# Optimization experiments

Measured on AMD Instinct MI355X. Metric: run time of the kernel, lower is better.

## Reference

```python
import jax, jax.numpy as jnp
import numpy as np

T, B, TD, HD, VD = 64, 4096, 512, 256, 484
LN_EPS = 1e-5   # torch nn.LayerNorm default
COS_EPS = 1e-8  # torch F.cosine_similarity default


def setup_inputs() -> dict:
    key = jax.random.key(0)
    ks = jax.random.split(key, 6)
    w = lambda k, shape: jax.random.normal(k, shape, dtype=jnp.float32) * 0.02
    return {
        "t_feat": jax.random.normal(ks[0], (B, TD), dtype=jnp.float32),
        "W1": w(ks[1], (T, HD, TD)),            # torch Linear weight layout [out, in]
        "b1": w(ks[2], (T, HD)),
        "gamma": jnp.ones((T, HD), jnp.float32),
        "beta": jnp.zeros((T, HD), jnp.float32),
        "W2": w(ks[3], (T, VD, HD)),
        "b2": w(ks[4], (T, VD)),
        "centroids": jax.random.normal(ks[5], (T, VD), dtype=jnp.float32),
    }


def reference(t_feat, W1, b1, gamma, beta, W2, b2, centroids):
    # All T per-task mappers batched into one grouped GEMM pipeline.
    # Linear1: [B, TD] x [T, HD, TD] -> [T, B, HD]
    h = jnp.einsum("bd,thd->tbh", t_feat, W1) + b1[:, None, :]
    # LayerNorm over hidden dim (per task affine params)
    mu = jnp.mean(h, axis=-1, keepdims=True)
    var = jnp.mean(jnp.square(h - mu), axis=-1, keepdims=True)
    h = (h - mu) * jax.lax.rsqrt(var + LN_EPS) * gamma[:, None, :] + beta[:, None, :]
    # Exact GELU (torch nn.GELU default uses erf)
    h = jax.nn.gelu(h, approximate=False)
    # Linear2: [T, B, HD] x [T, VD, HD] -> [T, B, VD] predicted visual features
    v = jnp.einsum("tbh,tvh->tbv", h, W2) + b2[:, None, :]
    # Cosine similarity vs each task centroid (eps-clamped norms, as in torch)
    v_norm = jnp.maximum(jnp.linalg.norm(v, axis=-1), COS_EPS)          # [T, B]
    c_norm = jnp.maximum(jnp.linalg.norm(centroids, axis=-1), COS_EPS)  # [T]
    cos = jnp.einsum("tbv,tv->tb", v, centroids) / (v_norm * c_norm[:, None])
    distances = jnp.mean(1.0 - cos, axis=-1)  # [T] mean cosine distance per task
    best_task = jnp.argmin(distances)          # top-1 routing decision
    return distances, best_task
```

## Files before the change

kernel.cpp:

```cpp
#include <hip/hip_runtime.h>
#include <math.h>

#define TASKS 64
#define NB    4096
#define TDI   512
#define HDI   256
#define VDI   484

#define WS_TF   ((size_t)0)
#define WS_W1   ((size_t)4194304)
#define WS_W2   ((size_t)20971520)
#define WS_CN   ((size_t)37748736)
#define WS_BC   ((size_t)37748992)
#define WS_ACC  ((size_t)37749248)

#define LDS_HP 0
#define LDS_B2 32768
#define LDS_R0 34816
#define LDS_R1 35840
#define LDS_MU 36864
#define LDS_RS 37120
#define SMEM_BYTES 37376

typedef _Float16 half8 __attribute__((ext_vector_type(8)));
typedef float    f32x4 __attribute__((ext_vector_type(4)));

#define MFMA16(a, b, c) __builtin_amdgcn_mfma_f32_16x16x32_f16((a), (b), (c), 0, 0, 0)

__device__ __forceinline__ float gelu_exact(float x) {
  float az = fabsf(x) * 0.70710678118654752f;
  float d  = fmaf(0.3275911f, az, 1.0f);
  float t; asm("v_rcp_f32 %0, %1" : "=v"(t) : "v"(d));
  float p  = fmaf(t, 1.061405429f, -1.453152027f);
  p = fmaf(t, p, 1.421413741f);
  p = fmaf(t, p, -0.284496736f);
  p = fmaf(t, p, 0.254829592f);
  p = p * t;
  float m = az * az * -1.4426950408889634f;
  float e; asm("v_exp_f32 %0, %1" : "=v"(e) : "v"(m));
  float er = fmaf(-p, e, 1.0f);
  er = copysignf(er, x);
  float hx = 0.5f * x;
  return fmaf(hx, er, hx);
}

extern "C" __global__ void prep_all(const float* __restrict__ t_feat,
                                    const float* __restrict__ W1,
                                    const float* __restrict__ W2,
                                    const float* __restrict__ b2,
                                    const float* __restrict__ cent,
                                    _Float16* __restrict__ tf,
                                    _Float16* __restrict__ w1,
                                    _Float16* __restrict__ w2,
                                    float* __restrict__ cnorm,
                                    float* __restrict__ bc,
                                    float* __restrict__ accum) {
  __shared__ __align__(16) char pbuf[17408];
  const int bid = blockIdx.x, tid = threadIdx.x;

  if (bid < 2304) {
    const float* src;
    half8* dst;
    int w2vdBase = -1;

    if (bid < 256) {
      int rb = bid >> 2, kq = bid & 3;
      src = t_feat + (size_t)rb * 64 * 512 + kq * 128;
      dst = (half8*)tf + ((size_t)rb * 4096 + kq * 1024);
    } else if (bid < 1280) {
      int g = bid - 256;
      int t = g >> 4, w_ = (g >> 2) & 3, kq = g & 3;
      src = W1 + ((size_t)t * 256 + w_ * 64) * 512 + kq * 128;
      dst = (half8*)w1 + ((size_t)t * 16384 + w_ * 4096 + kq * 1024);
    } else {
      int g = bid - 1280;
      int t = g >> 4, sub = g & 15;
      int p = sub >> 3, w_ = (sub >> 1) & 3, kq = sub & 1;
      src = W2 + (size_t)t * 484 * 256 + kq * 128;
      w2vdBase = p * 256 + w_ * 64;
      dst = (half8*)w2 + ((size_t)t * 16384 + p * 8192 + w_ * 2048 + kq * 1024);
    }

    const int srcStride = (w2vdBase < 0) ? 512 : 256;
    ushort* lds = (ushort*)pbuf;
    #pragma unroll
    for (int j = 0; j < 8; ++j) {
      int f = j * 256 + tid;
      int row = f >> 5, kc = f & 31;
      float4 v = make_float4(0.f, 0.f, 0.f, 0.f);
      if (w2vdBase < 0) {
        v = ((const float4*)(src + (size_t)row * srcStride))[kc];
      } else {
        int vd = w2vdBase + row;
        if (vd < VDI) v = ((const float4*)(src + (size_t)vd * 256))[kc];
      }
      _Float16 h4[4] = {(_Float16)v.x, (_Float16)v.y, (_Float16)v.z, (_Float16)v.w};
      *(ushort4*)(&lds[row * 136 + kc * 4]) = *(const ushort4*)h4;
    }
    __syncthreads();

    #pragma unroll
    for (int j = 0; j < 4; ++j) {
      int u = j * 256 + tid;
      int ksl = u >> 8, rg = (u >> 6) & 3, q = (u >> 4) & 3, l15 = u & 15;
      int row = rg * 16 + l15, k8l = ksl * 4 + q;
      half8 val = *(const half8*)(pbuf + row * 272 + k8l * 16);
      if (w2vdBase >= 0 && (w2vdBase + row) == VDI) continue;
      dst[u] = val;
    }
  } else {
    int t = bid - 2304;
    int h = tid;
    float* redc = (float*)pbuf;
    float* redb = (float*)(pbuf + 1024);
    float wcv = 0.f;
    for (int v = 0; v < VDI; ++v)
      wcv += W2[((size_t)t * VDI + v) * HDI + h] * cent[(size_t)t * VDI + v];
    {
      int ks = h >> 5, q = (h >> 3) & 3;
      size_t o = (size_t)t * 16384 + 8192 + 3 * 2048 + ks * 256 + 2 * 64 + q * 16 + 4;
      w2[o * 8 + (h & 7)] = (_Float16)wcv;
    }
    float c2 = 0.f, b2c = 0.f;
    for (int v = h; v < VDI; v += 256) {
      float c = cent[(size_t)t * VDI + v];
      c2 += c * c;
      b2c += b2[(size_t)t * VDI + v] * c;
    }
    redc[tid] = c2; redb[tid] = b2c;
    __syncthreads();
    if (tid < 64) {
      c2  = redc[tid] + redc[tid + 64] + redc[tid + 128] + redc[tid + 192];
      b2c = redb[tid] + redb[tid + 64] + redb[tid + 128] + redb[tid + 192];
      #pragma unroll
      for (int off = 32; off; off >>= 1) { c2 += __shfl_xor(c2, off); b2c += __shfl_xor(b2c, off); }
      if (tid == 0) { cnorm[t] = sqrtf(c2); bc[t] = b2c; accum[t] = 0.f; }
    }
  }
}


#define STEP_RELOAD(A, ACC, PB) do {                                           \
  __builtin_amdgcn_s_setprio(1);                                               \
  _Pragma("unroll") for (int ct_ = 0; ct_ < 4; ++ct_) {                        \
    ACC[0][ct_] = MFMA16(A[0], b[ct_], ACC[0][ct_]);                           \
    ACC[1][ct_] = MFMA16(A[1], b[ct_], ACC[1][ct_]);                           \
    ACC[2][ct_] = MFMA16(A[2], b[ct_], ACC[2][ct_]);                           \
    ACC[3][ct_] = MFMA16(A[3], b[ct_], ACC[3][ct_]);                           \
    b[ct_] = (PB)[ct_ * 64];                                                   \
  }                                                                            \
  __builtin_amdgcn_s_setprio(0);                                               \
} while (0)

#define STEP_LAST(A, ACC) do {                                                 \
  __builtin_amdgcn_s_setprio(1);                                               \
  _Pragma("unroll") for (int ct_ = 0; ct_ < 4; ++ct_) {                        \
    ACC[0][ct_] = MFMA16(A[0], b[ct_], ACC[0][ct_]);                           \
    ACC[1][ct_] = MFMA16(A[1], b[ct_], ACC[1][ct_]);                           \
    ACC[2][ct_] = MFMA16(A[2], b[ct_], ACC[2][ct_]);                           \
    ACC[3][ct_] = MFMA16(A[3], b[ct_], ACC[3][ct_]);                           \
  }                                                                            \
  __builtin_amdgcn_s_setprio(0);                                               \
} while (0)

#define LD_A4(D, P) do { D[0] = (P)[0]; D[1] = (P)[64]; D[2] = (P)[128]; D[3] = (P)[192]; } while (0)

#define P3_STEP(ACC, HN) do {                                                  \
  __builtin_amdgcn_s_setprio(1);                                               \
  ACC[0][0]=MFMA16(a0[0],b[0],ACC[0][0]); ACC[1][0]=MFMA16(a0[1],b[0],ACC[1][0]); \
  ACC[2][0]=MFMA16(a0[2],b[0],ACC[2][0]); ACC[3][0]=MFMA16(a0[3],b[0],ACC[3][0]); \
  b[0]=pc[0];                                                                  \
  ACC[0][1]=MFMA16(a0[0],b[1],ACC[0][1]); ACC[1][1]=MFMA16(a0[1],b[1],ACC[1][1]); \
  ACC[2][1]=MFMA16(a0[2],b[1],ACC[2][1]); ACC[3][1]=MFMA16(a0[3],b[1],ACC[3][1]); \
  b[1]=pc[64];                                                                 \
  ACC[0][2]=MFMA16(a0[0],b[2],ACC[0][2]); ACC[1][2]=MFMA16(a0[1],b[2],ACC[1][2]); \
  ACC[2][2]=MFMA16(a0[2],b[2],ACC[2][2]); ACC[3][2]=MFMA16(a0[3],b[2],ACC[3][2]); \
  b[2]=pc[128];                                                                \
  ACC[0][3]=MFMA16(a0[0],b[3],ACC[0][3]); a0[0]=*(const half8*)(HN);           \
  ACC[1][3]=MFMA16(a0[1],b[3],ACC[1][3]); a0[1]=*(const half8*)((HN)+1024);    \
  ACC[2][3]=MFMA16(a0[2],b[3],ACC[2][3]); a0[2]=*(const half8*)((HN)+2048);    \
  ACC[3][3]=MFMA16(a0[3],b[3],ACC[3][3]); a0[3]=*(const half8*)((HN)+3072);    \
  b[3]=pc[192]; pc+=256;                                                       \
  __builtin_amdgcn_s_setprio(0);                                               \
} while (0)

extern "C" __global__ void __launch_bounds__(256, 4)
router_main(const half8* __restrict__ tfv,
            const half8* __restrict__ w1v,
            const half8* __restrict__ w2v,
            const float* __restrict__ b1,
            const float* __restrict__ gamma,
            const float* __restrict__ beta,
            const float* __restrict__ b2,
            const float* __restrict__ bc,
            const float* __restrict__ cnorm,
            float* __restrict__ accum) {
  __shared__ __align__(16) char smem[SMEM_BYTES];

  const int tid = threadIdx.x;
  const int bx  = blockIdx.x;
  const int t  = ((bx & 7) << 3) | (bx >> 9);
  const int rb = (bx >> 3) & 63;

  const int lane = tid & 63;
  const int w    = tid >> 6;
  const int quad = lane >> 4;
  const int l15  = lane & 15;

  f32x4 zero4 = {0.f, 0.f, 0.f, 0.f};
  f32x4 acc[4][4];
  #pragma unroll
  for (int rt = 0; rt < 4; ++rt)
    #pragma unroll
    for (int ct = 0; ct < 4; ++ct) acc[rt][ct] = zero4;

  half8 a0[4], a1[4], b[4];

  {
    const half8* pa = tfv + ((size_t)rb * 4096 + quad * 16 + l15);
    const half8* pb = w1v + ((size_t)t * 16384 + w * 4096 + quad * 16 + l15);
    LD_A4(a0, pa);
    b[0] = pb[0]; b[1] = pb[64]; b[2] = pb[128]; b[3] = pb[192];
    a1[0] = pa[256]; a1[1] = pa[320]; a1[2] = pa[384]; a1[3] = pa[448];
    pa += 512;
    pb += 256;
    #pragma unroll 1
    for (int ks = 0; ks < 14; ks += 2) {
      STEP_RELOAD(a0, acc, pb); pb += 256;
      LD_A4(a0, pa);            pa += 256;
      STEP_RELOAD(a1, acc, pb); pb += 256;
      LD_A4(a1, pa);            pa += 256;
    }
    STEP_RELOAD(a0, acc, pb);
    STEP_LAST(a1, acc);
  }

  float b1v[4];
  #pragma unroll
  for (int ct = 0; ct < 4; ++ct)
    b1v[ct] = b1[t * HDI + w * 64 + ct * 16 + l15];
  {
    float* red0 = (float*)(smem + LDS_R0);
    float* red1 = (float*)(smem + LDS_R1);
    #pragma unroll
    for (int rt = 0; rt < 4; ++rt)
      #pragma unroll
      for (int r = 0; r < 4; ++r) {
        float sv = 0.f, qv = 0.f;
        #pragma unroll
        for (int ct = 0; ct < 4; ++ct) {
          float v = acc[rt][ct][r] + b1v[ct];
          acc[rt][ct][r] = v;
          sv += v; qv += v * v;
        }
        sv += __shfl_xor(sv, 1); qv += __shfl_xor(qv, 1);
        sv += __shfl_xor(sv, 2); qv += __shfl_xor(qv, 2);
        sv += __shfl_xor(sv, 4); qv += __shfl_xor(qv, 4);
        sv += __shfl_xor(sv, 8); qv += __shfl_xor(qv, 8);
        if (l15 == 0) {
          int m = rt * 16 + quad * 4 + r;
          red0[w * 64 + m] = sv;
          red1[w * 64 + m] = qv;
        }
      }
    __syncthreads();
    if (tid < 64) {
      float s = red0[tid] + red0[64 + tid] + red0[128 + tid] + red0[192 + tid];
      float q = red1[tid] + red1[64 + tid] + red1[128 + tid] + red1[192 + tid];
      float mu = s * (1.f / HDI);
      float var = q * (1.f / HDI) - mu * mu;
      ((float*)(smem + LDS_MU))[tid] = mu;
      ((float*)(smem + LDS_RS))[tid] = rsqrtf(var + 1e-5f);
    }
    float gvv[4], bevv[4];
    #pragma unroll
    for (int ct = 0; ct < 4; ++ct) {
      gvv[ct]  = gamma[t * HDI + w * 64 + ct * 16 + l15];
      bevv[ct] = beta [t * HDI + w * 64 + ct * 16 + l15];
    }
    {
      float* b2s = (float*)(smem + LDS_B2);
      int i0 = tid;
      b2s[i0] = (i0 < VDI) ? b2[(size_t)t * VDI + i0] : 0.f;
      int i1 = tid + 256;
      float v = 0.f;
      if (i1 < VDI) v = b2[(size_t)t * VDI + i1];
      else if (i1 == VDI) v = bc[t];
      b2s[i1] = v;
    }
    __syncthreads();
    const float* mus = (const float*)(smem + LDS_MU);
    const float* rss = (const float*)(smem + LDS_RS);
    #pragma unroll
    for (int rt = 0; rt < 4; ++rt) {
      float m4[4], s4[4];
      #pragma unroll
      for (int r = 0; r < 4; ++r) {
        int m = rt * 16 + quad * 4 + r;
        m4[r] = mus[m]; s4[r] = rss[m];
      }
      #pragma unroll
      for (int ct = 0; ct < 4; ++ct) {
        int col = w * 64 + ct * 16 + l15;
        int base = (((col >> 5) * 4 + rt) * 4 + ((col >> 3) & 3)) * 256
                 + quad * 64 + (l15 & 7) * 2;
        #pragma unroll
        for (int r = 0; r < 4; ++r) {
          float x = (acc[rt][ct][r] - m4[r]) * s4[r];
          x = x * gvv[ct] + bevv[ct];
          *(_Float16*)(smem + LDS_HP + base + r * 16) = (_Float16)gelu_exact(x);
        }
      }
    }
    __syncthreads();
  }

  {
    const float* b2s = (const float*)(smem + LDS_B2);
    float* red0 = (float*)(smem + LDS_R0);
    float* red1 = (float*)(smem + LDS_R1);
    const char* ha = smem + LDS_HP + quad * 256 + l15 * 16;

    #pragma unroll 1
    for (int pass = 0; pass < 2; ++pass) {
      const half8* pc = w2v + ((size_t)t * 16384 + pass * 8192 + w * 2048 + quad * 16 + l15);
      f32x4 acc2[4][4];
      #pragma unroll
      for (int rt = 0; rt < 4; ++rt)
        #pragma unroll
        for (int ct = 0; ct < 4; ++ct) acc2[rt][ct] = zero4;

      a0[0] = *(const half8*)(ha);        a0[1] = *(const half8*)(ha + 1024);
      a0[2] = *(const half8*)(ha + 2048); a0[3] = *(const half8*)(ha + 3072);
      b[0] = pc[0]; b[1] = pc[64]; b[2] = pc[128]; b[3] = pc[192];
      pc += 256;
      #pragma unroll 1
      for (int ks = 0; ks < 7; ++ks) {
        P3_STEP(acc2, ha + (ks + 1) * 4096);
      }
      STEP_LAST(a0, acc2);

      #pragma unroll
      for (int rt = 0; rt < 4; ++rt)
        #pragma unroll
        for (int r = 0; r < 4; ++r) {
          float ssq = 0.f, dtv = 0.f;
          #pragma unroll
          for (int ct = 0; ct < 4; ++ct) {
            int vcol = pass * 256 + w * 64 + ct * 16 + l15;
            float val = acc2[rt][ct][r] + b2s[vcol];
            ssq += (vcol < VDI) ? val * val : 0.f;
            dtv += (vcol == VDI) ? val : 0.f;
          }
          ssq += __shfl_xor(ssq, 1); dtv += __shfl_xor(dtv, 1);
          ssq += __shfl_xor(ssq, 2); dtv += __shfl_xor(dtv, 2);
          ssq += __shfl_xor(ssq, 4); dtv += __shfl_xor(dtv, 4);
          ssq += __shfl_xor(ssq, 8); dtv += __shfl_xor(dtv, 8);
          if (l15 == 0) {
            int m = rt * 16 + quad * 4 + r;
            if (pass == 0) {
              red0[w * 64 + m] = ssq;
            } else {
              red0[w * 64 + m] += ssq;
              red1[w * 64 + m] = dtv;
            }
          }
        }
    }

    __syncthreads();
    if (tid < 64) {
      float ss  = red0[tid] + red0[64 + tid] + red0[128 + tid] + red0[192 + tid];
      float dot = red1[tid] + red1[64 + tid] + red1[128 + tid] + red1[192 + tid];
      float cn = fmaxf(cnorm[t], 1e-8f);
      float vn = fmaxf(sqrtf(ss), 1e-8f);
      float part = 1.0f - dot / (vn * cn);
      part += __shfl_down(part, 32);
      part += __shfl_down(part, 16);
      part += __shfl_down(part, 8);
      part += __shfl_down(part, 4);
      part += __shfl_down(part, 2);
      part += __shfl_down(part, 1);
      if (tid == 0) atomicAdd(accum + t, part);
    }
  }
}

extern "C" __global__ void finalize_k(const float* __restrict__ accum, float* __restrict__ out) {
  int t = threadIdx.x;
  float d = accum[t] * (1.0f / (float)NB);
  out[t] = d;
  float bd = d; int bi = t;
  #pragma unroll
  for (int off = 32; off; off >>= 1) {
    float od = __shfl_xor(bd, off);
    int   oi = __shfl_xor(bi, off);
    if (od < bd || (od == bd && oi < bi)) { bd = od; bi = oi; }
  }
  if (t == 0) out[64] = (float)bi;
}

extern "C" void kernel_launch(void* const* d_in, const int* in_sizes, int n_in,
                              void* d_out, int out_size, void* d_ws, size_t ws_size,
                              hipStream_t stream) {
  const float* t_feat = (const float*)d_in[0];
  const float* W1     = (const float*)d_in[1];
  const float* b1     = (const float*)d_in[2];
  const float* gamma  = (const float*)d_in[3];
  const float* beta   = (const float*)d_in[4];
  const float* W2     = (const float*)d_in[5];
  const float* b2     = (const float*)d_in[6];
  const float* cent   = (const float*)d_in[7];

  char* ws = (char*)d_ws;
  _Float16* tf = (_Float16*)(ws + WS_TF);
  _Float16* w1 = (_Float16*)(ws + WS_W1);
  _Float16* w2 = (_Float16*)(ws + WS_W2);
  float* cnorm = (float*)(ws + WS_CN);
  float* bc    = (float*)(ws + WS_BC);
  float* accum = (float*)(ws + WS_ACC);
  float* out = (float*)d_out;

  prep_all<<<2368, 256, 0, stream>>>(t_feat, W1, W2, b2, cent,
                                     tf, w1, w2, cnorm, bc, accum);
  router_main<<<4096, 256, 0, stream>>>((const half8*)tf, (const half8*)w1, (const half8*)w2,
                                        b1, gamma, beta, b2, bc, cnorm, accum);
  finalize_k<<<1, 64, 0, stream>>>(accum, out);
}
```

Measured before the change: 317.9 us.

## Split W2·centroid reduction across blocks and prefetch W2 fragments earlier

The serial 484-step W2·centroid dot product that 64 blocks ran at the tail of the prep kernel is now split four ways across 256 blocks, each writing partial sums. A new small prep_fin kernel adds the partials, writes the folded column into the fp16 W2 layout, and computes the centroid norms and the bias-centroid dot. In the main kernel, the first W2 fragment loads are issued before the GELU epilogue, and the second pass's loads are issued before the first pass's reduction, to hide global load latency. The cost is one extra kernel launch and a workspace round trip for the partial sums.

Result: slower. 329.1 us (+3.5%).

```diff
diff --git a/kernel.cpp b/kernel.cpp
--- a/kernel.cpp
+++ b/kernel.cpp
@@ -13,6 +13,7 @@
 #define WS_CN   ((size_t)37748736)
 #define WS_BC   ((size_t)37748992)
 #define WS_ACC  ((size_t)37749248)
+#define WS_WCP  ((size_t)37749504)
 
 #define LDS_HP 0
 #define LDS_B2 32768
@@ -26,6 +27,13 @@
 typedef float    f32x4 __attribute__((ext_vector_type(4)));
 
 #define MFMA16(a, b, c) __builtin_amdgcn_mfma_f32_16x16x32_f16((a), (b), (c), 0, 0, 0)
+
+__device__ __forceinline__ half8 cvt8f(float4 v0, float4 v1) {
+  half8 r;
+  r[0]=(_Float16)v0.x; r[1]=(_Float16)v0.y; r[2]=(_Float16)v0.z; r[3]=(_Float16)v0.w;
+  r[4]=(_Float16)v1.x; r[5]=(_Float16)v1.y; r[6]=(_Float16)v1.z; r[7]=(_Float16)v1.w;
+  return r;
+}
 
 __device__ __forceinline__ float gelu_exact(float x) {
   float az = fabsf(x) * 0.70710678118654752f;
@@ -44,98 +52,120 @@
   return fmaf(hx, er, hx);
 }
 
-extern "C" __global__ void prep_all(const float* __restrict__ t_feat,
-                                    const float* __restrict__ W1,
-                                    const float* __restrict__ W2,
+extern "C" __global__ void __launch_bounds__(256, 8)
+prep_all(const float* __restrict__ t_feat,
+         const float* __restrict__ W1,
+         const float* __restrict__ W2,
+         const float* __restrict__ cent,
+         _Float16* __restrict__ tf,
+         _Float16* __restrict__ w1,
+         _Float16* __restrict__ w2,
+         float* __restrict__ wcp) {
+  __shared__ __align__(16) char pbuf[17408];
+  const int bid = blockIdx.x, tid = threadIdx.x;
+
+  if (bid < 256) {
+    int t = bid >> 2, q = bid & 3;
+    int h = tid;
+    int vs = q * 121;
+    const float* wp = W2 + ((size_t)t * VDI + vs) * HDI + h;
+    const float* cp = cent + (size_t)t * VDI + vs;
+    float s = 0.f;
+    int v = 0;
+    #pragma unroll 1
+    for (; v + 8 <= 121; v += 8) {
+      float x0 = wp[0 * 256], x1 = wp[1 * 256], x2 = wp[2 * 256], x3 = wp[3 * 256];
+      float x4 = wp[4 * 256], x5 = wp[5 * 256], x6 = wp[6 * 256], x7 = wp[7 * 256];
+      s = fmaf(x0, cp[v + 0], s); s = fmaf(x1, cp[v + 1], s);
+      s = fmaf(x2, cp[v + 2], s); s = fmaf(x3, cp[v + 3], s);
+      s = fmaf(x4, cp[v + 4], s); s = fmaf(x5, cp[v + 5], s);
+      s = fmaf(x6, cp[v + 6], s); s = fmaf(x7, cp[v + 7], s);
+      wp += 8 * 256;
+    }
+    s = fmaf(wp[0], cp[v], s);
+    wcp[((size_t)q * 64 + t) * 256 + h] = s;
+    return;
+  }
+
+  const float* src;
+  half8* dst;
+  int w2vdBase = -1;
+
+  if (bid < 512) {
+    int g = bid - 256;
+    int rb = g >> 2, kq = g & 3;
+    src = t_feat + (size_t)rb * 64 * 512 + kq * 128;
+    dst = (half8*)tf + ((size_t)rb * 4096 + kq * 1024);
+  } else if (bid < 1536) {
+    int g = bid - 512;
+    int t = g >> 4, w_ = (g >> 2) & 3, kq = g & 3;
+    src = W1 + ((size_t)t * 256 + w_ * 64) * 512 + kq * 128;
+    dst = (half8*)w1 + ((size_t)t * 16384 + w_ * 4096 + kq * 1024);
+  } else {
+    int g = bid - 1536;
+    int t = g >> 4, sub = g & 15;
+    int p = sub >> 3, w_ = (sub >> 1) & 3, kq = sub & 1;
+    src = W2 + (size_t)t * 484 * 256 + kq * 128;
+    w2vdBase = p * 256 + w_ * 64;
+    dst = (half8*)w2 + ((size_t)t * 16384 + p * 8192 + w_ * 2048 + kq * 1024);
+  }
+
+  const int srcStride = (w2vdBase < 0) ? 512 : 256;
+  ushort* lds = (ushort*)pbuf;
+  #pragma unroll
+  for (int j = 0; j < 8; ++j) {
+    int f = j * 256 + tid;
+    int row = f >> 5, kc = f & 31;
+    float4 v0 = make_float4(0.f, 0.f, 0.f, 0.f);
+    if (w2vdBase < 0) {
+      v0 = ((const float4*)(src + (size_t)row * srcStride))[kc];
+    } else {
+      int vd = w2vdBase + row;
+      if (vd < VDI) v0 = ((const float4*)(src + (size_t)vd * 256))[kc];
+    }
+    _Float16 h4[4] = {(_Float16)v0.x, (_Float16)v0.y, (_Float16)v0.z, (_Float16)v0.w};
+    *(ushort4*)(&lds[row * 136 + kc * 4]) = *(const ushort4*)h4;
+  }
+  __syncthreads();
+
+  #pragma unroll
+  for (int j = 0; j < 4; ++j) {
+    int u = j * 256 + tid;
+    int ksl = u >> 8, rg = (u >> 6) & 3, q = (u >> 4) & 3, l15 = u & 15;
+    int row = rg * 16 + l15, k8l = ksl * 4 + q;
+    dst[u] = *(const half8*)(pbuf + row * 272 + k8l * 16);
+  }
+}
+
+extern "C" __global__ void prep_fin(const float* __restrict__ wcp,
                                     const float* __restrict__ b2,
                                     const float* __restrict__ cent,
-                                    _Float16* __restrict__ tf,
-                                    _Float16* __restrict__ w1,
                                     _Float16* __restrict__ w2,
                                     float* __restrict__ cnorm,
                                     float* __restrict__ bc,
                                     float* __restrict__ accum) {
-  __shared__ __align__(16) char pbuf[17408];
-  const int bid = blockIdx.x, tid = threadIdx.x;
-
-  if (bid < 2304) {
-    const float* src;
-    half8* dst;
-    int w2vdBase = -1;
-
-    if (bid < 256) {
-      int rb = bid >> 2, kq = bid & 3;
-      src = t_feat + (size_t)rb * 64 * 512 + kq * 128;
-      dst = (half8*)tf + ((size_t)rb * 4096 + kq * 1024);
-    } else if (bid < 1280) {
-      int g = bid - 256;
-      int t = g >> 4, w_ = (g >> 2) & 3, kq = g & 3;
-      src = W1 + ((size_t)t * 256 + w_ * 64) * 512 + kq * 128;
-      dst = (half8*)w1 + ((size_t)t * 16384 + w_ * 4096 + kq * 1024);
-    } else {
-      int g = bid - 1280;
-      int t = g >> 4, sub = g & 15;
-      int p = sub >> 3, w_ = (sub >> 1) & 3, kq = sub & 1;
-      src = W2 + (size_t)t * 484 * 256 + kq * 128;
-      w2vdBase = p * 256 + w_ * 64;
-      dst = (half8*)w2 + ((size_t)t * 16384 + p * 8192 + w_ * 2048 + kq * 1024);
-    }
-
-    const int srcStride = (w2vdBase < 0) ? 512 : 256;
-    ushort* lds = (ushort*)pbuf;
+  __shared__ float redc[256], redb[256];
+  const int t = blockIdx.x, h = threadIdx.x;
+  float wc = wcp[((size_t)0 * 64 + t) * 256 + h] + wcp[((size_t)1 * 64 + t) * 256 + h]
+           + wcp[((size_t)2 * 64 + t) * 256 + h] + wcp[((size_t)3 * 64 + t) * 256 + h];
+  int ks = h >> 5, q = (h >> 3) & 3;
+  size_t o = (size_t)t * 16384 + 8192 + 3 * 2048 + ks * 256 + 2 * 64 + q * 16 + 4;
+  w2[o * 8 + (h & 7)] = (_Float16)wc;
+
+  float c2 = 0.f, b2c = 0.f;
+  for (int v = h; v < VDI; v += 256) {
+    float c = cent[(size_t)t * VDI + v];
+    c2 += c * c;
+    b2c += b2[(size_t)t * VDI + v] * c;
+  }
+  redc[h] = c2; redb[h] = b2c;
+  __syncthreads();
+  if (h < 64) {
+    c2  = redc[h] + redc[h + 64] + redc[h + 128] + redc[h + 192];
+    b2c = redb[h] + redb[h + 64] + redb[h + 128] + redb[h + 192];
     #pragma unroll
-    for (int j = 0; j < 8; ++j) {
-      int f = j * 256 + tid;
-      int row = f >> 5, kc = f & 31;
-      float4 v = make_float4(0.f, 0.f, 0.f, 0.f);
-      if (w2vdBase < 0) {
-        v = ((const float4*)(src + (size_t)row * srcStride))[kc];
-      } else {
-        int vd = w2vdBase + row;
-        if (vd < VDI) v = ((const float4*)(src + (size_t)vd * 256))[kc];
-      }
-      _Float16 h4[4] = {(_Float16)v.x, (_Float16)v.y, (_Float16)v.z, (_Float16)v.w};
-      *(ushort4*)(&lds[row * 136 + kc * 4]) = *(const ushort4*)h4;
-    }
-    __syncthreads();
-
-    #pragma unroll
-    for (int j = 0; j < 4; ++j) {
-      int u = j * 256 + tid;
-      int ksl = u >> 8, rg = (u >> 6) & 3, q = (u >> 4) & 3, l15 = u & 15;
-      int row = rg * 16 + l15, k8l = ksl * 4 + q;
-      half8 val = *(const half8*)(pbuf + row * 272 + k8l * 16);
-      if (w2vdBase >= 0 && (w2vdBase + row) == VDI) continue;
-      dst[u] = val;
-    }
-  } else {
-    int t = bid - 2304;
-    int h = tid;
-    float* redc = (float*)pbuf;
-    float* redb = (float*)(pbuf + 1024);
-    float wcv = 0.f;
-    for (int v = 0; v < VDI; ++v)
-      wcv += W2[((size_t)t * VDI + v) * HDI + h] * cent[(size_t)t * VDI + v];
-    {
-      int ks = h >> 5, q = (h >> 3) & 3;
-      size_t o = (size_t)t * 16384 + 8192 + 3 * 2048 + ks * 256 + 2 * 64 + q * 16 + 4;
-      w2[o * 8 + (h & 7)] = (_Float16)wcv;
-    }
-    float c2 = 0.f, b2c = 0.f;
-    for (int v = h; v < VDI; v += 256) {
-      float c = cent[(size_t)t * VDI + v];
-      c2 += c * c;
-      b2c += b2[(size_t)t * VDI + v] * c;
-    }
-    redc[tid] = c2; redb[tid] = b2c;
-    __syncthreads();
-    if (tid < 64) {
-      c2  = redc[tid] + redc[tid + 64] + redc[tid + 128] + redc[tid + 192];
-      b2c = redb[tid] + redb[tid + 64] + redb[tid + 128] + redb[tid + 192];
-      #pragma unroll
-      for (int off = 32; off; off >>= 1) { c2 += __shfl_xor(c2, off); b2c += __shfl_xor(b2c, off); }
-      if (tid == 0) { cnorm[t] = sqrtf(c2); bc[t] = b2c; accum[t] = 0.f; }
-    }
+    for (int off = 32; off; off >>= 1) { c2 += __shfl_xor(c2, off); b2c += __shfl_xor(b2c, off); }
+    if (h == 0) { cnorm[t] = sqrtf(c2); bc[t] = b2c; accum[t] = 0.f; }
   }
 }
 
@@ -289,6 +319,10 @@
       b2s[i1] = v;
     }
     __syncthreads();
+    {
+      const half8* p0 = w2v + ((size_t)t * 16384 + w * 2048 + quad * 16 + l15);
+      b[0] = p0[0]; b[1] = p0[64]; b[2] = p0[128]; b[3] = p0[192];
+    }
     const float* mus = (const float*)(smem + LDS_MU);
     const float* rss = (const float*)(smem + LDS_RS);
     #pragma unroll
@@ -320,10 +354,11 @@
     float* red0 = (float*)(smem + LDS_R0);
     float* red1 = (float*)(smem + LDS_R1);
     const char* ha = smem + LDS_HP + quad * 256 + l15 * 16;
+    const half8* pcb = w2v + ((size_t)t * 16384 + w * 2048 + quad * 16 + l15);
 
     #pragma unroll 1
     for (int pass = 0; pass < 2; ++pass) {
-      const half8* pc = w2v + ((size_t)t * 16384 + pass * 8192 + w * 2048 + quad * 16 + l15);
+      const half8* pc = pcb + pass * 8192 + 256;
       f32x4 acc2[4][4];
       #pragma unroll
       for (int rt = 0; rt < 4; ++rt)
@@ -332,13 +367,15 @@
 
       a0[0] = *(const half8*)(ha);        a0[1] = *(const half8*)(ha + 1024);
       a0[2] = *(const half8*)(ha + 2048); a0[3] = *(const half8*)(ha + 3072);
-      b[0] = pc[0]; b[1] = pc[64]; b[2] = pc[128]; b[3] = pc[192];
-      pc += 256;
       #pragma unroll 1
       for (int ks = 0; ks < 7; ++ks) {
         P3_STEP(acc2, ha + (ks + 1) * 4096);
       }
       STEP_LAST(a0, acc2);
+      if (pass == 0) {
+        const half8* pn = pcb + 8192;
+        b[0] = pn[0]; b[1] = pn[64]; b[2] = pn[128]; b[3] = pn[192];
+      }
 
       #pragma unroll
       for (int rt = 0; rt < 4; ++rt)
@@ -419,10 +456,11 @@
   float* cnorm = (float*)(ws + WS_CN);
   float* bc    = (float*)(ws + WS_BC);
   float* accum = (float*)(ws + WS_ACC);
+  float* wcp   = (float*)(ws + WS_WCP);
   float* out = (float*)d_out;
 
-  prep_all<<<2368, 256, 0, stream>>>(t_feat, W1, W2, b2, cent,
-                                     tf, w1, w2, cnorm, bc, accum);
+  prep_all<<<2560, 256, 0, stream>>>(t_feat, W1, W2, cent, tf, w1, w2, wcp);
+  prep_fin<<<64, 256, 0, stream>>>(wcp, b2, cent, w2, cnorm, bc, accum);
   router_main<<<4096, 256, 0, stream>>>((const half8*)tf, (const half8*)w1, (const half8*)w2,
                                         b1, gamma, beta, b2, bc, cnorm, accum);
   finalize_k<<<1, 64, 0, stream>>>(accum, out);
```
